# Kernel optimization log

Measured on AMD Instinct MI355X. Metric: run time of the kernel, lower is better.

The kernel has to match this reference:

```python
import jax, jax.numpy as jnp
import numpy as np

N = 50000      # nodes
E = 800000     # edges (avg degree 16)
F_IN = 128     # num_features
H = 64         # hidden_dim
G = 64         # graphs in batch


def setup_inputs() -> dict:
    key = jax.random.key(0)
    ks = jax.random.split(key, 20)
    inp = {
        "x": jax.random.normal(ks[0], (N, F_IN), jnp.float32),
        "edge_index": jax.random.randint(ks[1], (2, E), 0, N, dtype=jnp.int32).astype(jnp.int64),
        "batch": jnp.sort(jax.random.randint(ks[2], (N,), 0, G, dtype=jnp.int32)).astype(jnp.int64),
    }
    # GraphConv layer dims: in -> out
    dims = [(F_IN, H), (H, 2 * H), (2 * H, 3 * H), (3 * H, H)]
    k = 3
    for i, (din, dout) in enumerate(dims):
        s = 1.0 / np.sqrt(din).astype(np.float32)
        inp[f"w{i+1}_rel"] = jax.random.normal(ks[k], (din, dout), jnp.float32) * s
        inp[f"w{i+1}_root"] = jax.random.normal(ks[k + 1], (din, dout), jnp.float32) * s
        inp[f"b{i+1}"] = jnp.zeros((dout,), jnp.float32)
        k += 2
    inp["head_w"] = jax.random.normal(ks[k], (H, 1), jnp.float32) * (1.0 / np.sqrt(H).astype(np.float32))
    inp["head_b"] = jnp.zeros((1,), jnp.float32)
    return inp


def _graph_conv(x, src, dst, w_rel, w_root, b):
    # PyG GraphConv: out = lin_rel(sum_{j in N(i)} x_j) + lin_root(x_i)
    agg = jax.ops.segment_sum(x[src], dst, num_segments=N)  # [N, din]
    return agg @ w_rel + b + x @ w_root


def reference(x, edge_index, batch,
              w1_rel, w1_root, b1,
              w2_rel, w2_root, b2,
              w3_rel, w3_root, b3,
              w4_rel, w4_root, b4,
              head_w, head_b):
    src, dst = edge_index[0], edge_index[1]
    h = jax.nn.relu(_graph_conv(x, src, dst, w1_rel, w1_root, b1))
    h = jax.nn.relu(_graph_conv(h, src, dst, w2_rel, w2_root, b2))
    h = jax.nn.relu(_graph_conv(h, src, dst, w3_rel, w3_root, b3))
    h = _graph_conv(h, src, dst, w4_rel, w4_root, b4)          # [N, H]
    # global_mean_pool over graph ids
    sums = jax.ops.segment_sum(h, batch, num_segments=G)       # [G, H]
    counts = jax.ops.segment_sum(jnp.ones((N,), h.dtype), batch, num_segments=G)
    pooled = sums / jnp.maximum(counts, 1.0)[:, None]          # [G, H]
    return pooled @ head_w + head_b                            # [G, 1]
```

## Files before the change

kernel.cpp:

```cpp
#include <hip/hip_runtime.h>


#define NNODES 50000
#define NEDGES 800000
#define NGRAPH 64
#define NBUK 256
#define BSZ 196
#define EPB (NEDGES / NBUK)
#define CVT_NB (NNODES * 128 / 4 / 256)
#define PACK_NB (160 * 512 / 256)
#define RGRID ((NNODES + 127) / 128)
#define RCHUNK ((RGRID + 7) / 8)

typedef __attribute__((ext_vector_type(8))) __bf16 bf16x8;
typedef __attribute__((ext_vector_type(16))) float f32x16;

__device__ __forceinline__ unsigned short f2bf(float f) {
    unsigned u = __float_as_uint(f);
    u += 0x7fff + ((u >> 16) & 1);
    return (unsigned short)(u >> 16);
}
__device__ __forceinline__ float bf2f(unsigned b) {
    return __uint_as_float(b << 16);
}


__global__ void hist_kernel(const int* __restrict__ dst, int* __restrict__ cnt) {
    __shared__ int h[NBUK];
    int tid = threadIdx.x, k = blockIdx.x;
    h[tid] = 0;
    __syncthreads();
    int end = (k + 1) * EPB;
    for (int i = k * EPB + tid; i < end; i += 256)
        atomicAdd(&h[dst[i] / BSZ], 1);
    __syncthreads();
    cnt[tid * NBUK + k] = h[tid];
}

__global__ void scan1_kernel(int* __restrict__ a, int* __restrict__ bsum, int n) {
    __shared__ int buf[256];
    int tid = threadIdx.x;
    int i = blockIdx.x * 256 + tid;
    int v = (i < n) ? a[i] : 0;
    buf[tid] = v;
    __syncthreads();
    #pragma unroll
    for (int off = 1; off < 256; off <<= 1) {
        int t = (tid >= off) ? buf[tid - off] : 0;
        __syncthreads();
        buf[tid] += t;
        __syncthreads();
    }
    if (i < n) a[i] = buf[tid] - v;
    if (tid == 255) bsum[blockIdx.x] = buf[255];
}

__global__ void scan2_kernel(int* __restrict__ bsum, int nb) {
    __shared__ int buf[256];
    int tid = threadIdx.x;
    int v = (tid < nb) ? bsum[tid] : 0;
    buf[tid] = v;
    __syncthreads();
    #pragma unroll
    for (int off = 1; off < 256; off <<= 1) {
        int t = (tid >= off) ? buf[tid - off] : 0;
        __syncthreads();
        buf[tid] += t;
        __syncthreads();
    }
    if (tid < nb) bsum[tid] = buf[tid] - v;
}

__global__ void partition_kernel(const int* __restrict__ src, const int* __restrict__ dst,
                                 const int* __restrict__ cnt, const int* __restrict__ bsum,
                                 unsigned long long* __restrict__ pedge) {
    __shared__ int lbase[NBUK];
    int tid = threadIdx.x, k = blockIdx.x;
    lbase[tid] = cnt[tid * NBUK + k] + bsum[tid];
    __syncthreads();
    int end = (k + 1) * EPB;
    for (int i = k * EPB + tid; i < end; i += 256) {
        int s = src[i], d = dst[i];
        int pos = atomicAdd(&lbase[d / BSZ], 1);
        pedge[pos] = (unsigned long long)(unsigned)s | ((unsigned long long)(unsigned)d << 32);
    }
}

__global__ void build_kernel(const unsigned long long* __restrict__ pedge,
                             const int* __restrict__ bsum,
                             int* __restrict__ rp, int* __restrict__ csr) {
    __shared__ int sdeg[256], sc[256], sbase[256], sfill[256];
    int tid = threadIdx.x, b = blockIdx.x;
    int node0 = b * BSZ;
    int ncnt = NNODES - node0;
    if (ncnt > BSZ) ncnt = BSZ;
    if (ncnt < 0) ncnt = 0;
    int seg0 = bsum[b];
    int seg1 = (b + 1 < NBUK) ? bsum[b + 1] : NEDGES;
    sdeg[tid] = 0;
    sfill[tid] = 0;
    __syncthreads();
    for (int i = seg0 + tid; i < seg1; i += 256)
        atomicAdd(&sdeg[(int)(pedge[i] >> 32) - node0], 1);
    __syncthreads();
    sc[tid] = sdeg[tid];
    __syncthreads();
    #pragma unroll
    for (int off = 1; off < 256; off <<= 1) {
        int t = (tid >= off) ? sc[tid - off] : 0;
        __syncthreads();
        sc[tid] += t;
        __syncthreads();
    }
    sbase[tid] = sc[tid] - sdeg[tid];
    if (tid < ncnt) rp[node0 + tid] = seg0 + sbase[tid];
    if (b == NBUK - 1 && tid == 0) rp[NNODES] = NEDGES;
    __syncthreads();
    for (int i = seg0 + tid; i < seg1; i += 256) {
        unsigned long long p = pedge[i];
        int d = (int)(p >> 32) - node0;
        int pos = atomicAdd(&sfill[d], 1);
        csr[seg0 + sbase[d] + pos] = (int)(p & 0xffffffffu);
    }
}


__device__ __forceinline__ void pack32(const float* __restrict__ W, unsigned short* __restrict__ dst,
                                       int KS_tot, int ks0, int dcols, int ct0,
                                       int tl, int ksl, int lane, int j) {
    int k = ksl * 16 + ((lane >> 5) << 3) + j;
    int col = tl * 32 + (lane & 31);
    dst[(((size_t)(ct0 + tl) * KS_tot + (ks0 + ksl)) * 64 + lane) * 8 + j] = f2bf(W[k * dcols + col]);
}

__global__ void prep_kernel(const float* __restrict__ x, unsigned short* __restrict__ xbf,
                            const float* __restrict__ w1_rel, const float* __restrict__ w1_root,
                            const float* __restrict__ w2_rel, const float* __restrict__ w2_root,
                            const float* __restrict__ w3_rel, const float* __restrict__ w3_root,
                            unsigned short* __restrict__ pL1, unsigned short* __restrict__ pL2,
                            unsigned short* __restrict__ pL3,
                            const float* __restrict__ w4_rel, const float* __restrict__ w4_root,
                            const float* __restrict__ b4, const float* __restrict__ head_w,
                            float* __restrict__ wr, float* __restrict__ wt,
                            float* __restrict__ cbuf) {
    int b = blockIdx.x;
    int tid = threadIdx.x;
    if (b < CVT_NB) {
        int i = b * 256 + tid;
        float4 v = ((const float4*)x)[i];
        unsigned lo = (unsigned)f2bf(v.x) | ((unsigned)f2bf(v.y) << 16);
        unsigned hi = (unsigned)f2bf(v.z) | ((unsigned)f2bf(v.w) << 16);
        ((uint2*)xbf)[i] = make_uint2(lo, hi);
    } else if (b < CVT_NB + PACK_NB) {
        int idx = (b - CVT_NB) * 256 + tid;
        int g = idx >> 9;
        int t = idx & 511;
        int lane = (t >> 3) & 63, j = t & 7;
        if (g < 16)       { int gl = g;       pack32(w1_rel,  pL1, 8,  0, 64,  0, gl / 8, gl % 8, lane, j); }
        else if (g < 32)  { int gl = g - 16;  pack32(w1_root, pL1, 8,  0, 64,  2, gl / 8, gl % 8, lane, j); }
        else if (g < 48)  { int gl = g - 32;  pack32(w2_rel,  pL2, 8,  0, 128, 0, gl / 4, gl % 4, lane, j); }
        else if (g < 64)  { int gl = g - 48;  pack32(w2_root, pL2, 8,  4, 128, 0, gl / 4, gl % 4, lane, j); }
        else if (g < 112) { int gl = g - 64;  pack32(w3_rel,  pL3, 16, 0, 192, 0, gl / 8, gl % 8, lane, j); }
        else              { int gl = g - 112; pack32(w3_root, pL3, 16, 8, 192, 0, gl / 8, gl % 8, lane, j); }
    } else {
        if (tid < 192) {
            float ar = 0.f, at = 0.f;
            for (int j = 0; j < 64; j++) {
                float hw = head_w[j];
                ar = fmaf(w4_rel[tid * 64 + j], hw, ar);
                at = fmaf(w4_root[tid * 64 + j], hw, at);
            }
            wr[tid] = ar;
            wt[tid] = at;
        } else if (tid == 192) {
            float c = 0.f;
            for (int j = 0; j < 64; j++) c = fmaf(b4[j], head_w[j], c);
            cbuf[0] = c;
        }
    }
}


template<int KS, int NC>
__global__ __launch_bounds__(256, 4) void gemm_v4(
    const unsigned short* __restrict__ A, const unsigned short* __restrict__ W,
    const float* __restrict__ bias, unsigned short* __restrict__ OUT,
    int ldo, int ocol0, int relu, int N)
{
    const int K = KS * 16;
    int i = blockIdx.x;
    int chunk = i / (NC * 8);
    int rem = i - chunk * (NC * 8);
    int cg = rem >> 3;
    int rowb = chunk * 8 + (rem & 7);
    int tid = threadIdx.x;
    int wave = tid >> 6, lane = tid & 63;
    int l32 = lane & 31, half = lane >> 5;
    int rbase = rowb * 128 + wave * 32;
    if (rbase >= N) return;

    int arow = rbase + l32;
    if (arow >= N) arow = N - 1;
    const unsigned short* ap = A + (size_t)arow * K + half * 8;
    const unsigned short* wp = W + (size_t)cg * KS * 512 + lane * 8;

    f32x16 acc;
    #pragma unroll
    for (int r = 0; r < 16; r++) acc[r] = 0.f;

    #pragma unroll 1
    for (int kb = 0; kb < KS; kb += 8) {
        bf16x8 areg[8], breg[8];
        #pragma unroll
        for (int j = 0; j < 8; j++) {
            areg[j] = *(const bf16x8*)(ap + (kb + j) * 16);
            breg[j] = *(const bf16x8*)(wp + (size_t)(kb + j) * 512);
        }
        __builtin_amdgcn_sched_barrier(0);
        #pragma unroll
        for (int j = 0; j < 8; j++)
            acc = __builtin_amdgcn_mfma_f32_32x32x16_bf16(areg[j], breg[j], acc, 0, 0, 0);
    }

    int col = cg * 32 + l32;
    float bi = bias ? bias[col] : 0.f;
    #pragma unroll
    for (int reg = 0; reg < 16; reg++) {
        int row = rbase + (reg & 3) + 8 * (reg >> 2) + 4 * half;
        if (row < N) {
            float v = acc[reg] + bi;
            if (relu) v = fmaxf(v, 0.f);
            OUT[(size_t)row * ldo + ocol0 + col] = f2bf(v);
        }
    }
}


__device__ __forceinline__ void acc8(float* a, uint4 u) {
    a[0] += bf2f(u.x & 0xffffu); a[1] += bf2f(u.x >> 16);
    a[2] += bf2f(u.y & 0xffffu); a[3] += bf2f(u.y >> 16);
    a[4] += bf2f(u.z & 0xffffu); a[5] += bf2f(u.z >> 16);
    a[6] += bf2f(u.w & 0xffffu); a[7] += bf2f(u.w >> 16);
}

template<int LPF, int SUBS>
__global__ void agg_kernel_v3(const unsigned short* __restrict__ X, int ldx,
                              const int* __restrict__ rp, const int* __restrict__ csr,
                              const unsigned short* __restrict__ root, int ldr,
                              const float* __restrict__ bias, int relu,
                              unsigned short* __restrict__ OUT, int ldo, int N) {
    int t = blockIdx.x * blockDim.x + threadIdx.x;
    int node = t / (SUBS * LPF);
    int r = t % (SUBS * LPF);
    int sub = r / LPF;
    int sl = r % LPF;
    if (node >= N) return;
    float a[8] = {0.f, 0.f, 0.f, 0.f, 0.f, 0.f, 0.f, 0.f};
    int e0 = rp[node], e1 = rp[node + 1];
    const unsigned short* xb = X + 8 * sl;
    int e = e0 + sub;
    for (; e + SUBS < e1; e += 2 * SUBS) {
        int s0 = csr[e], s1 = csr[e + SUBS];
        uint4 u0 = *(const uint4*)(xb + (size_t)s0 * ldx);
        uint4 u1 = *(const uint4*)(xb + (size_t)s1 * ldx);
        acc8(a, u0);
        acc8(a, u1);
    }
    if (e < e1) {
        uint4 u = *(const uint4*)(xb + (size_t)csr[e] * ldx);
        acc8(a, u);
    }
    #pragma unroll
    for (int m = LPF; m < SUBS * LPF; m <<= 1)
        #pragma unroll
        for (int i = 0; i < 8; i++) a[i] += __shfl_xor(a[i], m, 64);
    if (sub == 0) {
        if (root) {
            uint4 u = *(const uint4*)(root + (size_t)node * ldr + 8 * sl);
            acc8(a, u);
        }
        if (bias) {
            float4 b0 = *(const float4*)(bias + 8 * sl);
            float4 b1 = *(const float4*)(bias + 8 * sl + 4);
            a[0] += b0.x; a[1] += b0.y; a[2] += b0.z; a[3] += b0.w;
            a[4] += b1.x; a[5] += b1.y; a[6] += b1.z; a[7] += b1.w;
        }
        if (relu) {
            #pragma unroll
            for (int i = 0; i < 8; i++) a[i] = fmaxf(a[i], 0.f);
        }
        uint4 o;
        o.x = (unsigned)f2bf(a[0]) | ((unsigned)f2bf(a[1]) << 16);
        o.y = (unsigned)f2bf(a[2]) | ((unsigned)f2bf(a[3]) << 16);
        o.z = (unsigned)f2bf(a[4]) | ((unsigned)f2bf(a[5]) << 16);
        o.w = (unsigned)f2bf(a[6]) | ((unsigned)f2bf(a[7]) << 16);
        *(uint4*)(OUT + (size_t)node * ldo + 8 * sl) = o;
    }
}


__global__ void st_kernel(const unsigned short* __restrict__ h3, const float* __restrict__ wr,
                          const float* __restrict__ wt, float* __restrict__ s,
                          float* __restrict__ t, int N) {
    int lane = threadIdx.x & 63;
    int node = (blockIdx.x * blockDim.x + threadIdx.x) >> 6;
    if (node >= N) return;
    float as = 0.f, at = 0.f;
    if (lane < 48) {
        uint2 u = *(const uint2*)(h3 + (size_t)node * 192 + 4 * lane);
        float x0 = bf2f(u.x & 0xffffu), x1 = bf2f(u.x >> 16);
        float x2 = bf2f(u.y & 0xffffu), x3 = bf2f(u.y >> 16);
        float4 r4 = *(const float4*)(wr + 4 * lane);
        float4 t4 = *(const float4*)(wt + 4 * lane);
        as = x0 * r4.x + x1 * r4.y + x2 * r4.z + x3 * r4.w;
        at = x0 * t4.x + x1 * t4.y + x2 * t4.z + x3 * t4.w;
    }
    #pragma unroll
    for (int off = 32; off > 0; off >>= 1) {
        as += __shfl_down(as, off, 64);
        at += __shfl_down(at, off, 64);
    }
    if (lane == 0) { s[node] = as; t[node] = at; }
}

__global__ void aggpool_kernel(const float* __restrict__ s, const float* __restrict__ t,
                               const int* __restrict__ rp, const int* __restrict__ csr,
                               const int* __restrict__ batch, float* __restrict__ gsum,
                               int* __restrict__ cnt, int* __restrict__ done,
                               const float* __restrict__ cbuf, const float* __restrict__ head_b,
                               float* __restrict__ out, int N) {
    __shared__ float ls[NGRAPH];
    __shared__ int lc[NGRAPH];
    __shared__ int lastflag;
    int tid = threadIdx.x;
    if (tid < NGRAPH) { ls[tid] = 0.f; lc[tid] = 0; }
    __syncthreads();
    int gidx = blockIdx.x * blockDim.x + tid;
    int node = gidx >> 2, sub = gidx & 3;
    if (node < N) {
        float a = 0.f;
        int e = rp[node] + sub, e1 = rp[node + 1];
        for (; e + 4 < e1; e += 8) a += s[csr[e]] + s[csr[e + 4]];
        if (e < e1) a += s[csr[e]];
        a += __shfl_xor(a, 1, 64);
        a += __shfl_xor(a, 2, 64);
        if (sub == 0) {
            int g = batch[node];
            atomicAdd(&ls[g], a + t[node]);
            atomicAdd(&lc[g], 1);
        }
    }
    __syncthreads();
    if (tid < NGRAPH && lc[tid] > 0) {
        atomicAdd(&gsum[tid], ls[tid]);
        atomicAdd(&cnt[tid], lc[tid]);
    }
    __syncthreads();
    if (tid == 0) {
        __threadfence();
        int d = atomicAdd(done, 1);
        lastflag = (d == (int)gridDim.x - 1);
    }
    __syncthreads();
    if (lastflag && tid < NGRAPH) {
        __threadfence();
        float gs = atomicAdd(&gsum[tid], 0.0f);
        int c = atomicAdd(&cnt[tid], 0);
        float cc = (float)(c > 0 ? c : 1);
        out[tid] = gs / cc + cbuf[0] + head_b[0];
    }
}


extern "C" void kernel_launch(void* const* d_in, const int* in_sizes, int n_in,
                              void* d_out, int out_size, void* d_ws, size_t ws_size,
                              hipStream_t stream) {
    const float* x       = (const float*)d_in[0];
    const int*   edge    = (const int*)d_in[1];
    const int*   batch   = (const int*)d_in[2];
    const float* w1_rel  = (const float*)d_in[3];
    const float* w1_root = (const float*)d_in[4];
    const float* b1      = (const float*)d_in[5];
    const float* w2_rel  = (const float*)d_in[6];
    const float* w2_root = (const float*)d_in[7];
    const float* b2      = (const float*)d_in[8];
    const float* w3_rel  = (const float*)d_in[9];
    const float* w3_root = (const float*)d_in[10];
    const float* b3      = (const float*)d_in[11];
    const float* w4_rel  = (const float*)d_in[12];
    const float* w4_root = (const float*)d_in[13];
    const float* b4      = (const float*)d_in[14];
    const float* head_w  = (const float*)d_in[15];
    const float* head_b  = (const float*)d_in[16];
    float* out = (float*)d_out;

    const int N = NNODES, E = NEDGES;
    const int* src = edge;
    const int* dst = edge + E;

    char* ws = (char*)d_ws;
    size_t off = 0;
    auto alloc = [&](size_t bytes) -> char* {
        char* p = ws + off;
        off = (off + bytes + 255) & ~(size_t)255;
        return p;
    };
    float* gsum  = (float*)alloc(NGRAPH * 4);
    int*   cnt   = (int*)alloc(NGRAPH * 4);
    int*   done  = (int*)alloc(4);
    size_t zero_bytes = off;
    int*   bcnt  = (int*)alloc((size_t)NBUK * NBUK * 4);
    int*   bsum  = (int*)alloc(256 * 4);
    int*   rp    = (int*)alloc((size_t)(N + 1) * 4);
    int*   csr   = (int*)alloc((size_t)E * 4);
    unsigned long long* pedge = (unsigned long long*)alloc((size_t)E * 8);
    unsigned short* xbf    = (unsigned short*)alloc((size_t)N * 128 * 2);
    unsigned short* z1     = (unsigned short*)alloc((size_t)N * 128 * 2);
    unsigned short* combo2 = (unsigned short*)alloc((size_t)N * 128 * 2);
    unsigned short* combo3 = (unsigned short*)alloc((size_t)N * 256 * 2);
    unsigned short* h3     = (unsigned short*)alloc((size_t)N * 192 * 2);
    unsigned short* pL1    = (unsigned short*)alloc(4 * 8 * 512 * 2);
    unsigned short* pL2    = (unsigned short*)alloc(4 * 8 * 512 * 2);
    unsigned short* pL3    = (unsigned short*)alloc(6 * 16 * 512 * 2);
    float* sbuf  = (float*)alloc((size_t)N * 4);
    float* tbuf  = (float*)alloc((size_t)N * 4);
    float* wr    = (float*)alloc(192 * 4);
    float* wt    = (float*)alloc(192 * 4);
    float* cbuf  = (float*)alloc(4);
    (void)ws_size;

    hipMemsetAsync(gsum, 0, zero_bytes, stream);

    const int TB = 256;

    hist_kernel<<<NBUK, 256, 0, stream>>>(dst, bcnt);
    scan1_kernel<<<NBUK, 256, 0, stream>>>(bcnt, bsum, NBUK * NBUK);
    scan2_kernel<<<1, 256, 0, stream>>>(bsum, NBUK);
    partition_kernel<<<NBUK, 256, 0, stream>>>(src, dst, bcnt, bsum, pedge);
    build_kernel<<<NBUK, 256, 0, stream>>>(pedge, bsum, rp, csr);

    prep_kernel<<<CVT_NB + PACK_NB + 1, 256, 0, stream>>>(
        x, xbf, w1_rel, w1_root, w2_rel, w2_root, w3_rel, w3_root,
        pL1, pL2, pL3, w4_rel, w4_root, b4, head_w, wr, wt, cbuf);

    gemm_v4<8, 4><<<RCHUNK * 8 * 4, 256, 0, stream>>>(xbf, pL1, nullptr, z1, 128, 0, 0, N);
    agg_kernel_v3<8, 4><<<(N * 32 + TB - 1) / TB, TB, 0, stream>>>(z1, 128, rp, csr,
                                                                   z1 + 64, 128, b1, 1, combo2 + 64, 128, N);
    agg_kernel_v3<8, 4><<<(N * 32 + TB - 1) / TB, TB, 0, stream>>>(combo2 + 64, 128, rp, csr,
                                                                   nullptr, 0, nullptr, 0, combo2, 128, N);
    gemm_v4<8, 4><<<RCHUNK * 8 * 4, 256, 0, stream>>>(combo2, pL2, b2, combo3, 256, 128, 1, N);
    agg_kernel_v3<16, 4><<<(N * 64 + TB - 1) / TB, TB, 0, stream>>>(combo3 + 128, 256, rp, csr,
                                                                    nullptr, 0, nullptr, 0, combo3, 256, N);
    gemm_v4<16, 6><<<RCHUNK * 8 * 6, 256, 0, stream>>>(combo3, pL3, b3, h3, 192, 0, 1, N);

    st_kernel<<<(N * 64 + TB - 1) / TB, TB, 0, stream>>>(h3, wr, wt, sbuf, tbuf, N);
    aggpool_kernel<<<(N * 4 + TB - 1) / TB, TB, 0, stream>>>(sbuf, tbuf, rp, csr, batch,
                                                             gsum, cnt, done, cbuf, head_b, out, N);
}
```

Baseline: 291.4 us.

## Fuse layer-4 head projection into layer-3 GEMM epilogue, dropping h3 buffer

```diff
diff --git a/kernel.cpp b/kernel.cpp
--- a/kernel.cpp
+++ b/kernel.cpp
@@ -181,11 +181,13 @@
 }
 
 
-template<int KS, int NC>
+template<int KS, int NC, int ST>
 __global__ __launch_bounds__(256, 4) void gemm_v4(
     const unsigned short* __restrict__ A, const unsigned short* __restrict__ W,
     const float* __restrict__ bias, unsigned short* __restrict__ OUT,
-    int ldo, int ocol0, int relu, int N)
+    int ldo, int ocol0, int relu, int N,
+    const float* __restrict__ wrp, const float* __restrict__ wtp,
+    float* __restrict__ sb, float* __restrict__ tb)
 {
     const int K = KS * 16;
     int i = blockIdx.x;
@@ -216,7 +218,6 @@
             areg[j] = *(const bf16x8*)(ap + (kb + j) * 16);
             breg[j] = *(const bf16x8*)(wp + (size_t)(kb + j) * 512);
         }
-        __builtin_amdgcn_sched_barrier(0);
         #pragma unroll
         for (int j = 0; j < 8; j++)
             acc = __builtin_amdgcn_mfma_f32_32x32x16_bf16(areg[j], breg[j], acc, 0, 0, 0);
@@ -224,13 +225,33 @@
 
     int col = cg * 32 + l32;
     float bi = bias ? bias[col] : 0.f;
-    #pragma unroll
-    for (int reg = 0; reg < 16; reg++) {
-        int row = rbase + (reg & 3) + 8 * (reg >> 2) + 4 * half;
-        if (row < N) {
-            float v = acc[reg] + bi;
-            if (relu) v = fmaxf(v, 0.f);
-            OUT[(size_t)row * ldo + ocol0 + col] = f2bf(v);
+    if constexpr (ST) {
+        float wrv = wrp[col], wtv = wtp[col];
+        #pragma unroll
+        for (int reg = 0; reg < 16; reg++) {
+            int row = rbase + (reg & 3) + 8 * (reg >> 2) + 4 * half;
+            float v = fmaxf(acc[reg] + bi, 0.f);
+            float sv = v * wrv;
+            float tv = v * wtv;
+            #pragma unroll
+            for (int m = 1; m < 32; m <<= 1) {
+                sv += __shfl_xor(sv, m, 64);
+                tv += __shfl_xor(tv, m, 64);
+            }
+            if (l32 == 0 && row < N) {
+                atomicAdd(&sb[row], sv);
+                atomicAdd(&tb[row], tv);
+            }
+        }
+    } else {
+        #pragma unroll
+        for (int reg = 0; reg < 16; reg++) {
+            int row = rbase + (reg & 3) + 8 * (reg >> 2) + 4 * half;
+            if (row < N) {
+                float v = acc[reg] + bi;
+                if (relu) v = fmaxf(v, 0.f);
+                OUT[(size_t)row * ldo + ocol0 + col] = f2bf(v);
+            }
         }
     }
 }
@@ -299,30 +320,6 @@
 }
 
 
-__global__ void st_kernel(const unsigned short* __restrict__ h3, const float* __restrict__ wr,
-                          const float* __restrict__ wt, float* __restrict__ s,
-                          float* __restrict__ t, int N) {
-    int lane = threadIdx.x & 63;
-    int node = (blockIdx.x * blockDim.x + threadIdx.x) >> 6;
-    if (node >= N) return;
-    float as = 0.f, at = 0.f;
-    if (lane < 48) {
-        uint2 u = *(const uint2*)(h3 + (size_t)node * 192 + 4 * lane);
-        float x0 = bf2f(u.x & 0xffffu), x1 = bf2f(u.x >> 16);
-        float x2 = bf2f(u.y & 0xffffu), x3 = bf2f(u.y >> 16);
-        float4 r4 = *(const float4*)(wr + 4 * lane);
-        float4 t4 = *(const float4*)(wt + 4 * lane);
-        as = x0 * r4.x + x1 * r4.y + x2 * r4.z + x3 * r4.w;
-        at = x0 * t4.x + x1 * t4.y + x2 * t4.z + x3 * t4.w;
-    }
-    #pragma unroll
-    for (int off = 32; off > 0; off >>= 1) {
-        as += __shfl_down(as, off, 64);
-        at += __shfl_down(at, off, 64);
-    }
-    if (lane == 0) { s[node] = as; t[node] = at; }
-}
-
 __global__ void aggpool_kernel(const float* __restrict__ s, const float* __restrict__ t,
                                const int* __restrict__ rp, const int* __restrict__ csr,
                                const int* __restrict__ batch, float* __restrict__ gsum,
@@ -408,6 +405,8 @@
     float* gsum  = (float*)alloc(NGRAPH * 4);
     int*   cnt   = (int*)alloc(NGRAPH * 4);
     int*   done  = (int*)alloc(4);
+    float* sbuf  = (float*)alloc((size_t)N * 4);
+    float* tbuf  = (float*)alloc((size_t)N * 4);
     size_t zero_bytes = off;
     int*   bcnt  = (int*)alloc((size_t)NBUK * NBUK * 4);
     int*   bsum  = (int*)alloc(256 * 4);
@@ -418,12 +417,9 @@
     unsigned short* z1     = (unsigned short*)alloc((size_t)N * 128 * 2);
     unsigned short* combo2 = (unsigned short*)alloc((size_t)N * 128 * 2);
     unsigned short* combo3 = (unsigned short*)alloc((size_t)N * 256 * 2);
-    unsigned short* h3     = (unsigned short*)alloc((size_t)N * 192 * 2);
     unsigned short* pL1    = (unsigned short*)alloc(4 * 8 * 512 * 2);
     unsigned short* pL2    = (unsigned short*)alloc(4 * 8 * 512 * 2);
     unsigned short* pL3    = (unsigned short*)alloc(6 * 16 * 512 * 2);
-    float* sbuf  = (float*)alloc((size_t)N * 4);
-    float* tbuf  = (float*)alloc((size_t)N * 4);
     float* wr    = (float*)alloc(192 * 4);
     float* wt    = (float*)alloc(192 * 4);
     float* cbuf  = (float*)alloc(4);
@@ -443,17 +439,19 @@
         x, xbf, w1_rel, w1_root, w2_rel, w2_root, w3_rel, w3_root,
         pL1, pL2, pL3, w4_rel, w4_root, b4, head_w, wr, wt, cbuf);
 
-    gemm_v4<8, 4><<<RCHUNK * 8 * 4, 256, 0, stream>>>(xbf, pL1, nullptr, z1, 128, 0, 0, N);
+    gemm_v4<8, 4, 0><<<RCHUNK * 8 * 4, 256, 0, stream>>>(xbf, pL1, nullptr, z1, 128, 0, 0, N,
+                                                         nullptr, nullptr, nullptr, nullptr);
     agg_kernel_v3<8, 4><<<(N * 32 + TB - 1) / TB, TB, 0, stream>>>(z1, 128, rp, csr,
                                                                    z1 + 64, 128, b1, 1, combo2 + 64, 128, N);
     agg_kernel_v3<8, 4><<<(N * 32 + TB - 1) / TB, TB, 0, stream>>>(combo2 + 64, 128, rp, csr,
                                                                    nullptr, 0, nullptr, 0, combo2, 128, N);
-    gemm_v4<8, 4><<<RCHUNK * 8 * 4, 256, 0, stream>>>(combo2, pL2, b2, combo3, 256, 128, 1, N);
+    gemm_v4<8, 4, 0><<<RCHUNK * 8 * 4, 256, 0, stream>>>(combo2, pL2, b2, combo3, 256, 128, 1, N,
+                                                         nullptr, nullptr, nullptr, nullptr);
     agg_kernel_v3<16, 4><<<(N * 64 + TB - 1) / TB, TB, 0, stream>>>(combo3 + 128, 256, rp, csr,
                                                                     nullptr, 0, nullptr, 0, combo3, 256, N);
-    gemm_v4<16, 6><<<RCHUNK * 8 * 6, 256, 0, stream>>>(combo3, pL3, b3, h3, 192, 0, 1, N);
-
-    st_kernel<<<(N * 64 + TB - 1) / TB, TB, 0, stream>>>(h3, wr, wt, sbuf, tbuf, N);
+    gemm_v4<16, 6, 1><<<RCHUNK * 8 * 6, 256, 0, stream>>>(combo3, pL3, b3, nullptr, 0, 0, 0, N,
+                                                          wr, wt, sbuf, tbuf);
+
     aggpool_kernel<<<(N * 4 + TB - 1) / TB, TB, 0, stream>>>(sbuf, tbuf, rp, csr, batch,
                                                              gsum, cnt, done, cbuf, head_b, out, N);
 }
```

After: 288.3 us. About the same (-1.1%).
